# Optimization experiments

Hardware: AMD Instinct MI355X
Metric: run time of the kernel (lower is better)

The kernel has to match this reference:

```python
import jax, jax.numpy as jnp
import numpy as np

D_MODEL = 256
H = 4              # hardcoded in the torch module via repeat(1,4,1)
DIM = D_MODEL // H # 64
N = 4096


def _conv1x1(x, W, b):
    # torch Conv1d(kernel_size=1): [B, Cin, N] -> [B, Cout, N]
    return jnp.einsum('oi,bin->bon', W, x) + b[None, :, None]


def setup_inputs() -> dict:
    key = jax.random.key(0)
    ks = jax.random.split(key, 13)
    s = 0.02
    inp = {
        'query':   jax.random.normal(ks[0], (1, D_MODEL, N), dtype=jnp.float32),
        'key':     jax.random.normal(ks[1], (1, D_MODEL, N), dtype=jnp.float32),
        'value':   jax.random.normal(ks[2], (1, D_MODEL, N), dtype=jnp.float32),
        'coords0': jax.random.normal(ks[3], (1, 3, N), dtype=jnp.float32),
        'coords1': jax.random.normal(ks[4], (1, 3, N), dtype=jnp.float32),
        'Wq': jax.random.normal(ks[5], (D_MODEL, D_MODEL), dtype=jnp.float32) * s,
        'bq': jnp.zeros((D_MODEL,), dtype=jnp.float32),
        'Wk': jax.random.normal(ks[6], (D_MODEL, D_MODEL), dtype=jnp.float32) * s,
        'bk': jnp.zeros((D_MODEL,), dtype=jnp.float32),
        'Wv': jax.random.normal(ks[7], (D_MODEL, D_MODEL), dtype=jnp.float32) * s,
        'bv': jnp.zeros((D_MODEL,), dtype=jnp.float32),
        'Wm': jax.random.normal(ks[8], (D_MODEL + 28, D_MODEL + 28), dtype=jnp.float32) * s,
        'bm': jnp.zeros((D_MODEL + 28,), dtype=jnp.float32),
    }
    return inp


def reference(query, key, value, coords0, coords1, Wq, bq, Wk, bk, Wv, bv, Wm, bm):
    B = query.shape[0]  # must be 1 (hardcoded in original via view(1,4,3,-1))
    Nq = coords0.shape[2]
    Nk = coords1.shape[2]

    # 1x1-conv projections, then split channels into (dim, heads): view(B, dim, H, N)
    q = _conv1x1(query, Wq, bq).reshape(B, DIM, H, Nq)
    k = _conv1x1(key,   Wk, bk).reshape(B, DIM, H, Nk)
    v = _conv1x1(value, Wv, bv).reshape(B, DIM, H, Nk)

    # coords1.repeat(1,4,1).view(1,4,3,-1).transpose(1,2) == broadcast coords over heads
    c1 = jnp.broadcast_to(coords1[:, :, None, :], (B, 3, H, Nk))
    v = jnp.concatenate([v, c1], axis=1)  # [B, DIM+3, H, Nk]

    # attention: scale is query.shape[1]**0.5 == DIM**0.5 (per-head dim)
    scores = jnp.einsum('bdhn,bdhm->bhnm', q, k) / jnp.asarray(DIM, q.dtype) ** 0.5
    prob = jax.nn.softmax(scores, axis=-1)          # [B, H, Nq, Nk]
    x = jnp.einsum('bhnm,bdhm->bdhn', prob, v)      # [B, DIM+3, H, Nq]

    # coordinate augmentation
    c0 = jnp.broadcast_to(coords0[:, :, None, :], (B, 3, H, Nq))
    aug1 = x[:, DIM:DIM + 3] - c0                   # [B, 3, H, Nq]
    aug2 = jnp.linalg.norm(aug1, axis=1, keepdims=True)  # [B, 1, H, Nq]

    y = jnp.concatenate([x, aug1, aug2], axis=1)    # [B, DIM+7, H, Nq]
    y = y.reshape(B, (DIM + 7) * H, Nq)
    return _conv1x1(y, Wm, bm)                      # [B, d_model+28, Nq]
```

## Files before the change

### kernel.cpp

```cpp
#include <hip/hip_runtime.h>
#include <hip/hip_bf16.h>

#define NN 4096

typedef __attribute__((ext_vector_type(8))) short short8;
typedef __attribute__((ext_vector_type(4))) float f32x4;

__device__ __forceinline__ unsigned short f2bf(float f) {
  union { float f; unsigned u; } v; v.f = f;
  unsigned u = v.u;
  u += 0x7fffu + ((u >> 16) & 1u);
  return (unsigned short)(u >> 16);
}

__device__ __forceinline__ unsigned packpair(float a, float b) {
  __hip_bfloat162 h = __float22bfloat162_rn(make_float2(a, b));
  union { __hip_bfloat162 h; unsigned u; } cv; cv.h = h;
  return cv.u;
}

__global__ __launch_bounds__(256) void transpose3_kernel(
    const float* __restrict__ q, const float* __restrict__ k, const float* __restrict__ v,
    unsigned short* __restrict__ Xt, const float* __restrict__ coords1,
    unsigned short* __restrict__ Vb) {
  __shared__ float Tl[64][65];
  const float* X = (blockIdx.z == 0) ? q : (blockIdx.z == 1) ? k : v;
  unsigned short* dst = Xt + (size_t)blockIdx.z * NN * 256;
  const int n0 = blockIdx.x << 6, k0 = blockIdx.y << 6;
  const int t = threadIdx.x;
  const int r = t >> 4, c4 = (t & 15) << 2;
#pragma unroll
  for (int i = 0; i < 4; ++i) {
    const float4 vv = *(const float4*)(X + (size_t)(k0 + r + 16 * i) * NN + n0 + c4);
    Tl[r + 16 * i][c4] = vv.x; Tl[r + 16 * i][c4 + 1] = vv.y;
    Tl[r + 16 * i][c4 + 2] = vv.z; Tl[r + 16 * i][c4 + 3] = vv.w;
  }
  __syncthreads();
  const int kc = (t & 7) << 3;
#pragma unroll
  for (int j = 0; j < 2; ++j) {
    const int n = (t >> 3) + (j << 5);
    unsigned pk[4];
#pragma unroll
    for (int u = 0; u < 4; ++u)
      pk[u] = packpair(Tl[kc + 2 * u][n], Tl[kc + 2 * u + 1][n]);
    *(uint4*)(dst + (size_t)(n0 + n) * 256 + k0 + kc) = *(uint4*)pk;
  }
  if (blockIdx.z == 2 && blockIdx.y == 0) {
    const int rr = t >> 2, seg = t & 3;
    const int h = rr >> 4, d = 64 + (rr & 15);
    unsigned short* vd = Vb + (size_t)(h * 80 + d) * NN + n0 + seg * 16;
    if (d < 67) {
      const float* src = coords1 + (size_t)(d - 64) * NN + n0 + seg * 16;
      unsigned u[8];
#pragma unroll
      for (int i = 0; i < 4; ++i) {
        const float4 cv = *(const float4*)(src + 4 * i);
        u[2 * i] = packpair(cv.x, cv.y);
        u[2 * i + 1] = packpair(cv.z, cv.w);
      }
      *(uint4*)vd = *(uint4*)&u[0];
      *(uint4*)(vd + 8) = *(uint4*)&u[4];
    } else {
      const uint4 zz = make_uint4(0u, 0u, 0u, 0u);
      *(uint4*)vd = zz;
      *(uint4*)(vd + 8) = zz;
    }
  }
}

__global__ __launch_bounds__(256) void proj_gemm_kernel(
    const float* __restrict__ Wq, const float* __restrict__ bq,
    const float* __restrict__ Wk, const float* __restrict__ bk,
    const float* __restrict__ Wv, const float* __restrict__ bv,
    const unsigned short* __restrict__ Xt,
    unsigned short* __restrict__ Qb, unsigned short* __restrict__ Kb,
    unsigned short* __restrict__ Vb) {
  __shared__ __align__(16) unsigned char smem[16384];
  __shared__ float Bls[64];
  const int z = blockIdx.z;
  const float* W  = (z == 0) ? Wq : (z == 1) ? Wk : Wv;
  const float* bb = (z == 0) ? bq : (z == 1) ? bk : bv;
  const unsigned short* Xz = Xt + (size_t)z * NN * 256;
  const int co0 = blockIdx.y << 6;
  const int n0 = blockIdx.x << 6;
  const int tid = threadIdx.x;
  const int w = tid >> 6, l = tid & 63;
  const int wm = w >> 1, wn = w & 1;
  const int c = l & 15, g = l >> 4;
  char* const Al = (char*)smem;
  char* const Bl = (char*)smem + 8192;

  if (tid < 64) Bls[tid] = bb[co0 + tid];

  const int ar = tid >> 2, ac = (tid & 3) << 4;
  const int br = tid >> 3, bch = tid & 7;
  const int aswz = (ar & 7) << 4;
  const int bswz = (br & 7) << 4;

  float4 wa[4];
  uint4 wb[2];
  f32x4 acc[2][2];
#pragma unroll
  for (int mf = 0; mf < 2; ++mf)
#pragma unroll
    for (int nf = 0; nf < 2; ++nf) acc[mf][nf] = (f32x4){0.f, 0.f, 0.f, 0.f};

#define PJ_LOAD(k0_) do { \
  _Pragma("unroll") for (int i = 0; i < 4; ++i) \
    wa[i] = *(const float4*)(W + (size_t)(co0 + ar) * 256 + (k0_) + ac + 4 * i); \
  wb[0] = *(const uint4*)(Xz + (size_t)(n0 + br) * 256 + (k0_) + bch * 8); \
  wb[1] = *(const uint4*)(Xz + (size_t)(n0 + br + 32) * 256 + (k0_) + bch * 8); \
} while (0)

#define PJ_STORE() do { \
  unsigned pk[8]; \
  _Pragma("unroll") for (int i = 0; i < 4; ++i) { \
    pk[2 * i] = packpair(wa[i].x, wa[i].y); \
    pk[2 * i + 1] = packpair(wa[i].z, wa[i].w); \
  } \
  *(uint4*)(Al + ar * 128 + (((ac << 1)) ^ aswz)) = *(uint4*)&pk[0]; \
  *(uint4*)(Al + ar * 128 + (((ac << 1) + 16) ^ aswz)) = *(uint4*)&pk[4]; \
  *(uint4*)(Bl + br * 128 + ((bch << 4) ^ bswz)) = wb[0]; \
  *(uint4*)(Bl + (br + 32) * 128 + ((bch << 4) ^ bswz)) = wb[1]; \
} while (0)

  PJ_LOAD(0);
  PJ_STORE();
  __syncthreads();

  for (int s = 0; s < 4; ++s) {
    const bool hav = (s + 1 < 4);
    if (hav) PJ_LOAD((s + 1) << 6);
    __builtin_amdgcn_s_setprio(1);
#pragma unroll
    for (int ks = 0; ks < 2; ++ks) {
      short8 af[2], bf[2];
#pragma unroll
      for (int mf = 0; mf < 2; ++mf) {
        const int row = wm * 32 + mf * 16 + c;
        af[mf] = *(const short8*)(Al + row * 128 + (((ks << 6) + (g << 4)) ^ ((row & 7) << 4)));
      }
#pragma unroll
      for (int nf = 0; nf < 2; ++nf) {
        const int row = wn * 32 + nf * 16 + c;
        bf[nf] = *(const short8*)(Bl + row * 128 + (((ks << 6) + (g << 4)) ^ ((row & 7) << 4)));
      }
#pragma unroll
      for (int mf = 0; mf < 2; ++mf)
#pragma unroll
        for (int nf = 0; nf < 2; ++nf)
          acc[mf][nf] = __builtin_amdgcn_mfma_f32_16x16x32_bf16(af[mf], bf[nf], acc[mf][nf], 0, 0, 0);
    }
    __builtin_amdgcn_s_setprio(0);
    __syncthreads();
    if (hav) {
      PJ_STORE();
      __syncthreads();
    }
  }

  unsigned short* Clu = (unsigned short*)smem;
  const float scale = (z == 0) ? 0.125f : 1.0f;
#pragma unroll
  for (int mf = 0; mf < 2; ++mf)
#pragma unroll
    for (int nf = 0; nf < 2; ++nf)
#pragma unroll
      for (int rr = 0; rr < 4; ++rr) {
        const int row = wm * 32 + mf * 16 + (g << 2) + rr;
        const int col = wn * 32 + nf * 16 + c;
        Clu[row * 72 + col] = f2bf((acc[mf][nf][rr] + Bls[row]) * scale);
      }
  __syncthreads();
  if (z <= 1) {
    unsigned short* Ob = (z == 0) ? Qb : Kb;
    const int d0 = co0 >> 2;
    const int h = tid >> 6, n = tid & 63;
    unsigned u[8];
#pragma unroll
    for (int p = 0; p < 8; ++p)
      u[p] = (unsigned)Clu[((p << 3) + h) * 72 + n] |
             ((unsigned)Clu[((p << 3) + 4 + h) * 72 + n] << 16);
    uint4* dd = (uint4*)(Ob + ((size_t)h * NN + n0 + n) * 64 + d0);
    dd[0] = *(uint4*)&u[0];
    dd[1] = *(uint4*)&u[4];
  } else {
    const int rl = tid >> 2, seg = (tid & 3) << 4;
    const int h = rl & 3, d = (co0 >> 2) + (rl >> 2);
    unsigned short* vd = Vb + (size_t)(h * 80 + d) * NN + n0 + seg;
    *(uint4*)vd = *(const uint4*)((char*)Clu + rl * 144 + (seg << 1));
    *(uint4*)(vd + 8) = *(const uint4*)((char*)Clu + rl * 144 + (seg << 1) + 16);
  }
}

__global__ __launch_bounds__(256) void attn_kernel(
    const unsigned short* __restrict__ Qb, const unsigned short* __restrict__ Kb,
    const unsigned short* __restrict__ Vb, float* __restrict__ Opart, int chunkKeys) {
  __shared__ __align__(16) unsigned char smem[34816];
  const int h = blockIdx.y;
  const int sp = blockIdx.z;
  const int qbase = blockIdx.x * 128;
  const int tid = threadIdx.x;
  const int w = tid >> 6;
  const int l = tid & 63;
  const int c = l & 15;
  const int g = l >> 4;
  const int swc = (c & 7) << 4;

  char* const Kls = (char*)smem;
  char* const Vls = (char*)smem + 8192;
  char* const Pls = (char*)smem + 18432 + w * 4096;

  short8 qf[2][2];
#pragma unroll
  for (int qs = 0; qs < 2; ++qs) {
    const unsigned short* qsrc = Qb + (((h * NN) + qbase + w * 32 + qs * 16 + c) << 6) + (g << 3);
    qf[qs][0] = *(const short8*)qsrc;
    qf[qs][1] = *(const short8*)(qsrc + 32);
  }

  f32x4 Of[2][5];
#pragma unroll
  for (int qs = 0; qs < 2; ++qs)
#pragma unroll
    for (int dt = 0; dt < 5; ++dt) Of[qs][dt] = (f32x4){0.f, 0.f, 0.f, 0.f};
  float mrun[2] = {-1e30f, -1e30f};
  float lrun[2] = {0.f, 0.f};

  const int r0 = tid >> 3, ch = tid & 7;
  const int so = (ch << 4) ^ ((r0 & 7) << 4);
  const int mStart = sp * chunkKeys;
  const int niter = chunkKeys >> 6;

  {
    const unsigned short* kbase = Kb + ((h * NN + mStart) << 6);
    const unsigned short* vbase = Vb + (size_t)(h * 80) * NN + mStart;
    const uint4 ka  = *(const uint4*)(kbase + (r0 << 6) + (ch << 3));
    const uint4 kb2 = *(const uint4*)(kbase + ((r0 + 32) << 6) + (ch << 3));
    const uint4 va  = *(const uint4*)(vbase + (size_t)r0 * NN + (ch << 3));
    const uint4 vb2 = *(const uint4*)(vbase + (size_t)(r0 + 32) * NN + (ch << 3));
    *(uint4*)(Kls + r0 * 128 + so) = ka;
    *(uint4*)(Kls + (r0 + 32) * 128 + so) = kb2;
    *(uint4*)(Vls + r0 * 128 + so) = va;
    *(uint4*)(Vls + (r0 + 32) * 128 + so) = vb2;
    if (tid < 128) {
      const uint4 vc = *(const uint4*)(vbase + (size_t)(r0 + 64) * NN + (ch << 3));
      *(uint4*)(Vls + (r0 + 64) * 128 + so) = vc;
    }
  }
  __syncthreads();

  for (int it = 0; it < niter; ++it) {
    uint4 ka, kb2, va, vb2, vc;
    const bool hav = (it + 1 < niter);
    if (hav) {
      const int m0 = mStart + ((it + 1) << 6);
      const unsigned short* kbase = Kb + ((h * NN + m0) << 6);
      const unsigned short* vbase = Vb + (size_t)(h * 80) * NN + m0;
      ka  = *(const uint4*)(kbase + (r0 << 6) + (ch << 3));
      kb2 = *(const uint4*)(kbase + ((r0 + 32) << 6) + (ch << 3));
      va  = *(const uint4*)(vbase + (size_t)r0 * NN + (ch << 3));
      vb2 = *(const uint4*)(vbase + (size_t)(r0 + 32) * NN + (ch << 3));
      if (tid < 128) vc = *(const uint4*)(vbase + (size_t)(r0 + 64) * NN + (ch << 3));
    }

    f32x4 sD[2][4];
    __builtin_amdgcn_s_setprio(1);
#pragma unroll
    for (int t = 0; t < 4; ++t) {
      const char* rp = Kls + (t * 16 + c) * 128;
      const short8 ka0 = *(const short8*)(rp + ((g << 4) ^ swc));
      const short8 ka1 = *(const short8*)(rp + ((64 + (g << 4)) ^ swc));
#pragma unroll
      for (int qs = 0; qs < 2; ++qs) {
        f32x4 a = (f32x4){0.f, 0.f, 0.f, 0.f};
        a = __builtin_amdgcn_mfma_f32_16x16x32_bf16(ka0, qf[qs][0], a, 0, 0, 0);
        a = __builtin_amdgcn_mfma_f32_16x16x32_bf16(ka1, qf[qs][1], a, 0, 0, 0);
        sD[qs][t] = a;
      }
    }
    __builtin_amdgcn_s_setprio(0);

#pragma unroll
    for (int qs = 0; qs < 2; ++qs) {
      float m01 = fmaxf(fmaxf(sD[qs][0][0], sD[qs][0][1]), fmaxf(sD[qs][0][2], sD[qs][0][3]));
      float m11 = fmaxf(fmaxf(sD[qs][1][0], sD[qs][1][1]), fmaxf(sD[qs][1][2], sD[qs][1][3]));
      float m21 = fmaxf(fmaxf(sD[qs][2][0], sD[qs][2][1]), fmaxf(sD[qs][2][2], sD[qs][2][3]));
      float m31 = fmaxf(fmaxf(sD[qs][3][0], sD[qs][3][1]), fmaxf(sD[qs][3][2], sD[qs][3][3]));
      float mx = fmaxf(fmaxf(m01, m11), fmaxf(m21, m31));
      mx = fmaxf(mx, __shfl_xor(mx, 16));
      mx = fmaxf(mx, __shfl_xor(mx, 32));
      if (!__all(mx - mrun[qs] <= 8.f)) {
        const float mnew = fmaxf(mrun[qs], mx);
        const float a = __expf(mrun[qs] - mnew);
        mrun[qs] = mnew;
        lrun[qs] *= a;
#pragma unroll
        for (int dt = 0; dt < 5; ++dt)
#pragma unroll
          for (int r = 0; r < 4; ++r) Of[qs][dt][r] *= a;
      }
      const float mm = mrun[qs];
      float rs = 0.f;
      unsigned pk[8];
#pragma unroll
      for (int t = 0; t < 4; ++t) {
        const float e0 = __expf(sD[qs][t][0] - mm);
        const float e1 = __expf(sD[qs][t][1] - mm);
        const float e2 = __expf(sD[qs][t][2] - mm);
        const float e3 = __expf(sD[qs][t][3] - mm);
        rs += (e0 + e1) + (e2 + e3);
        pk[t * 2]     = packpair(e0, e1);
        pk[t * 2 + 1] = packpair(e2, e3);
      }
      rs += __shfl_xor(rs, 16);
      rs += __shfl_xor(rs, 32);
      lrun[qs] += rs;
      char* prow = Pls + (qs * 16 + c) * 128;
#pragma unroll
      for (int t = 0; t < 4; ++t)
        *(uint2*)(prow + ((t * 32 + (g << 3)) ^ swc)) = make_uint2(pk[t * 2], pk[t * 2 + 1]);
    }

    short8 pb[2][2];
#pragma unroll
    for (int qs = 0; qs < 2; ++qs) {
      const char* prow = Pls + (qs * 16 + c) * 128;
      pb[qs][0] = *(const short8*)(prow + ((g << 4) ^ swc));
      pb[qs][1] = *(const short8*)(prow + ((64 + (g << 4)) ^ swc));
    }
    __builtin_amdgcn_s_setprio(1);
#pragma unroll
    for (int dt = 0; dt < 5; ++dt) {
      const char* vp = Vls + (dt * 16 + c) * 128;
      const short8 va0 = *(const short8*)(vp + ((g << 4) ^ swc));
      const short8 va1 = *(const short8*)(vp + ((64 + (g << 4)) ^ swc));
#pragma unroll
      for (int qs = 0; qs < 2; ++qs) {
        Of[qs][dt] = __builtin_amdgcn_mfma_f32_16x16x32_bf16(va0, pb[qs][0], Of[qs][dt], 0, 0, 0);
        Of[qs][dt] = __builtin_amdgcn_mfma_f32_16x16x32_bf16(va1, pb[qs][1], Of[qs][dt], 0, 0, 0);
      }
    }
    __builtin_amdgcn_s_setprio(0);

    __syncthreads();
    if (hav) {
      *(uint4*)(Kls + r0 * 128 + so) = ka;
      *(uint4*)(Kls + (r0 + 32) * 128 + so) = kb2;
      *(uint4*)(Vls + r0 * 128 + so) = va;
      *(uint4*)(Vls + (r0 + 32) * 128 + so) = vb2;
      if (tid < 128) *(uint4*)(Vls + (r0 + 64) * 128 + so) = vc;
    }
    __syncthreads();
  }

  const int rowbase = (sp * 4 + h) * 69;
#pragma unroll
  for (int qs = 0; qs < 2; ++qs) {
    const int qg = qbase + w * 32 + qs * 16 + c;
#pragma unroll
    for (int dt = 0; dt < 5; ++dt)
#pragma unroll
      for (int r = 0; r < 4; ++r) {
        const int dv = dt * 16 + (g << 2) + r;
        if (dv < 67) Opart[(size_t)(rowbase + dv) * NN + qg] = Of[qs][dt][r];
      }
    if (g == 0) {
      Opart[(size_t)(rowbase + 67) * NN + qg] = mrun[qs];
      Opart[(size_t)(rowbase + 68) * NN + qg] = lrun[qs];
    }
  }
}

template <int NS>
__global__ __launch_bounds__(256) void combine_t_kernel(
    const float* __restrict__ Opart, const float* __restrict__ coords0,
    unsigned short* __restrict__ Yt) {
  __shared__ __align__(16) unsigned char Yl[16 * 640];
  const int t = threadIdx.x;
  const int q = t & 15;
  const int worker = t >> 4;
  const int h = worker & 3;
  const int dgrp = worker >> 2;
  const int q0 = blockIdx.x << 4;
  const int qg = q0 + q;
  const int rowb = q * 640;
  const int sw = (q & 7) << 4;

  float m[NS], wgt[NS], lv[NS];
  float M = -1e30f;
#pragma unroll
  for (int s = 0; s < NS; ++s)
    m[s] = Opart[((size_t)(s * 4 + h) * 69 + 67) * NN + qg];
#pragma unroll
  for (int s = 0; s < NS; ++s)
    lv[s] = Opart[((size_t)(s * 4 + h) * 69 + 68) * NN + qg];
#pragma unroll
  for (int s = 0; s < NS; ++s) M = fmaxf(M, m[s]);
  float L = 0.f;
#pragma unroll
  for (int s = 0; s < NS; ++s) {
    wgt[s] = __expf(m[s] - M);
    L += lv[s] * wgt[s];
  }
  const float invL = 1.f / L;
#pragma unroll
  for (int s = 0; s < NS; ++s) wgt[s] *= invL;

  if (worker == 0) *(uint2*)(Yl + rowb + (568 ^ sw)) = make_uint2(0u, 0u);

  const int dv0 = dgrp * 17;
  const int dv1 = (dgrp == 3) ? 67 : dv0 + 17;
  float ss = 0.f;
#pragma unroll 2
  for (int dv = dv0; dv < dv1; ++dv) {
    float vals[NS];
#pragma unroll
    for (int s = 0; s < NS; ++s)
      vals[s] = Opart[((size_t)(s * 4 + h) * 69 + dv) * NN + qg];
    float a = 0.f;
#pragma unroll
    for (int s = 0; s < NS; ++s) a += vals[s] * wgt[s];
    *(unsigned short*)(Yl + rowb + ((((dv << 2) + h) << 1) ^ sw)) = f2bf(a);
    if (dv >= 64) {
      const float au = a - coords0[(size_t)(dv - 64) * NN + qg];
      *(unsigned short*)(Yl + rowb + (((((dv + 3) << 2) + h) << 1) ^ sw)) = f2bf(au);
      ss += au * au;
    }
  }
  if (dgrp == 3) *(unsigned short*)(Yl + rowb + (((280 + h) << 1) ^ sw)) = f2bf(sqrtf(ss));
  __syncthreads();

  for (int i = t; i < 16 * 36; i += 256) {
    const int row = i / 36, seg = i - row * 36;
    *(uint4*)(Yt + (size_t)(q0 + row) * 288 + (seg << 3)) =
        *(const uint4*)(Yl + row * 640 + ((seg << 4) ^ ((row & 7) << 4)));
  }
}

#define OP_LOAD(k0_) do { \
  const int arow = co0 + ar; \
  _Pragma("unroll") for (int i = 0; i < 6; ++i) { \
    const int col = (k0_) + ac + 4 * i; \
    wa[i] = (arow < 284 && col < 284) ? *(const float4*)(Wm + (size_t)arow * 284 + col) \
                                      : make_float4(0.f, 0.f, 0.f, 0.f); \
  } \
  _Pragma("unroll") for (int i = 0; i < 6; ++i) \
    wb[i] = *(const uint4*)(Yt + (size_t)(n0 + bn) * 288 + (k0_) + bc + 8 * i); \
} while (0)

#define OP_WRITE_LDS() do { \
  unsigned pk[12]; \
  _Pragma("unroll") for (int i = 0; i < 6; ++i) { \
    pk[2 * i] = packpair(wa[i].x, wa[i].y); \
    pk[2 * i + 1] = packpair(wa[i].z, wa[i].w); \
  } \
  _Pragma("unroll") for (int i = 0; i < 3; ++i) \
    *(uint4*)(Al + ar * 256 + (((ac << 1) + (i << 4)) ^ aswz)) = *(uint4*)&pk[4 * i]; \
  _Pragma("unroll") for (int i = 0; i < 6; ++i) \
    *(uint4*)(Bl + bn * 256 + (((bc << 1) + (i << 4)) ^ bswz)) = wb[i]; \
} while (0)

__global__ __launch_bounds__(256) void outproj_gemm_kernel(
    const unsigned short* __restrict__ Yt, const float* __restrict__ Wm,
    const float* __restrict__ bm, float* __restrict__ out) {
  __shared__ __align__(16) unsigned char smem[49152];
  __shared__ float Bls[64];
  const int co0 = blockIdx.y << 6;
  const int n0 = blockIdx.x << 7;
  const int tid = threadIdx.x;
  const int w = tid >> 6, l = tid & 63;
  const int wm = w >> 1, wn = w & 1;
  const int c = l & 15, g = l >> 4;
  char* const Al = (char*)smem;
  char* const Bl = (char*)smem + 16384;

  if (tid < 64) { const int co = co0 + tid; Bls[tid] = (co < 284) ? bm[co] : 0.f; }

  const int ar = tid >> 2, ac = (tid & 3) * 24;
  const int bn = tid >> 1, bc = (tid & 1) * 48;
  const int aswz = (ar & 7) << 4;
  const int bswz = (bn & 7) << 4;

  float4 wa[6];
  uint4 wb[6];
  f32x4 acc[2][4];
#pragma unroll
  for (int mf = 0; mf < 2; ++mf)
#pragma unroll
    for (int nf = 0; nf < 4; ++nf) acc[mf][nf] = (f32x4){0.f, 0.f, 0.f, 0.f};

  OP_LOAD(0);
  OP_WRITE_LDS();
  __syncthreads();

  for (int s = 0; s < 3; ++s) {
    const bool hav = (s + 1 < 3);
    if (hav) OP_LOAD((s + 1) * 96);
    __builtin_amdgcn_s_setprio(1);
#pragma unroll
    for (int ks = 0; ks < 3; ++ks) {
      short8 af[2], bf[4];
#pragma unroll
      for (int mf = 0; mf < 2; ++mf) {
        const int row = wm * 32 + mf * 16 + c;
        af[mf] = *(const short8*)(Al + row * 256 + (((ks << 6) + (g << 4)) ^ ((row & 7) << 4)));
      }
#pragma unroll
      for (int nf = 0; nf < 4; ++nf) {
        const int row = wn * 64 + nf * 16 + c;
        bf[nf] = *(const short8*)(Bl + row * 256 + (((ks << 6) + (g << 4)) ^ ((row & 7) << 4)));
      }
#pragma unroll
      for (int mf = 0; mf < 2; ++mf)
#pragma unroll
        for (int nf = 0; nf < 4; ++nf)
          acc[mf][nf] = __builtin_amdgcn_mfma_f32_16x16x32_bf16(af[mf], bf[nf], acc[mf][nf], 0, 0, 0);
    }
    __builtin_amdgcn_s_setprio(0);
    __syncthreads();
    if (hav) {
      OP_WRITE_LDS();
      __syncthreads();
    }
  }

#pragma unroll
  for (int mf = 0; mf < 2; ++mf)
#pragma unroll
    for (int nf = 0; nf < 4; ++nf)
#pragma unroll
      for (int rr = 0; rr < 4; ++rr) {
        const int row = wm * 32 + mf * 16 + (g << 2) + rr;
        const int co = co0 + row;
        if (co < 284)
          out[(size_t)co * NN + n0 + wn * 64 + nf * 16 + c] = acc[mf][nf][rr] + Bls[row];
      }
}

extern "C" void kernel_launch(void* const* d_in, const int* in_sizes, int n_in,
                              void* d_out, int out_size, void* d_ws, size_t ws_size,
                              hipStream_t stream) {
  const float* query   = (const float*)d_in[0];
  const float* key_    = (const float*)d_in[1];
  const float* value   = (const float*)d_in[2];
  const float* coords0 = (const float*)d_in[3];
  const float* coords1 = (const float*)d_in[4];
  const float* Wq = (const float*)d_in[5];
  const float* bq = (const float*)d_in[6];
  const float* Wk = (const float*)d_in[7];
  const float* bk = (const float*)d_in[8];
  const float* Wv = (const float*)d_in[9];
  const float* bv = (const float*)d_in[10];
  const float* Wm = (const float*)d_in[11];
  const float* bm = (const float*)d_in[12];
  float* out = (float*)d_out;

  unsigned short* Qb = (unsigned short*)d_ws;
  unsigned short* Kb = Qb + (size_t)4 * NN * 64;
  unsigned short* Vb = Kb + (size_t)4 * NN * 64;
  unsigned short* Xt = Vb + (size_t)4 * 80 * NN;
  unsigned short* Yt = Xt + (size_t)3 * NN * 256;
  float* Opart = (float*)(Yt + (size_t)NN * 288);

  const size_t fixedB = (size_t)((char*)Opart - (char*)d_ws);
  const size_t per = (size_t)4 * 69 * NN * 4;
  int nsplit = 8;
  while (nsplit > 1 && ws_size < fixedB + (size_t)nsplit * per) nsplit >>= 1;

  hipLaunchKernelGGL(transpose3_kernel, dim3(64, 4, 3), dim3(256), 0, stream,
                     query, key_, value, Xt, coords1, Vb);
  hipLaunchKernelGGL(proj_gemm_kernel, dim3(64, 4, 3), dim3(256), 0, stream,
                     Wq, bq, Wk, bk, Wv, bv, Xt, Qb, Kb, Vb);
  hipLaunchKernelGGL(attn_kernel, dim3(32, 4, nsplit), dim3(256), 0, stream,
                     Qb, Kb, Vb, Opart, NN / nsplit);
  switch (nsplit) {
    case 8:
      hipLaunchKernelGGL((combine_t_kernel<8>), dim3(256), dim3(256), 0, stream, Opart, coords0, Yt);
      break;
    case 4:
      hipLaunchKernelGGL((combine_t_kernel<4>), dim3(256), dim3(256), 0, stream, Opart, coords0, Yt);
      break;
    case 2:
      hipLaunchKernelGGL((combine_t_kernel<2>), dim3(256), dim3(256), 0, stream, Opart, coords0, Yt);
      break;
    default:
      hipLaunchKernelGGL((combine_t_kernel<1>), dim3(256), dim3(256), 0, stream, Opart, coords0, Yt);
      break;
  }
  hipLaunchKernelGGL(outproj_gemm_kernel, dim3(32, 5), dim3(256), 0, stream, Yt, Wm, bm, out);
}
```

Before: 93.47 us.

## Double-buffer attention K/V tiles, use exp2 softmax, shrink out-proj tile

The attention kernel now alternates between two LDS buffers for its K/V tiles. This removes one __syncthreads per iteration but raises shared memory per block, which may cut occupancy. The softmax folds log2(e) into the Q scale and uses the hardware exp2 instruction in place of __expf, with the rescale threshold widened to match the base-2 units. The output projection GEMM tile width is halved to 64 columns, doubling the grid so more blocks run across CUs.

```diff
diff --git a/kernel.cpp b/kernel.cpp
--- a/kernel.cpp
+++ b/kernel.cpp
@@ -161,7 +161,7 @@
   }
 
   unsigned short* Clu = (unsigned short*)smem;
-  const float scale = (z == 0) ? 0.125f : 1.0f;
+  const float scale = (z == 0) ? 0.18033688f : 1.0f;
 #pragma unroll
   for (int mf = 0; mf < 2; ++mf)
 #pragma unroll
@@ -197,7 +197,7 @@
 __global__ __launch_bounds__(256) void attn_kernel(
     const unsigned short* __restrict__ Qb, const unsigned short* __restrict__ Kb,
     const unsigned short* __restrict__ Vb, float* __restrict__ Opart, int chunkKeys) {
-  __shared__ __align__(16) unsigned char smem[34816];
+  __shared__ __align__(16) unsigned char smem[53248];
   const int h = blockIdx.y;
   const int sp = blockIdx.z;
   const int qbase = blockIdx.x * 128;
@@ -208,9 +208,7 @@
   const int g = l >> 4;
   const int swc = (c & 7) << 4;
 
-  char* const Kls = (char*)smem;
-  char* const Vls = (char*)smem + 8192;
-  char* const Pls = (char*)smem + 18432 + w * 4096;
+  char* const Pls = (char*)smem + 36864 + w * 4096;
 
   short8 qf[2][2];
 #pragma unroll
@@ -234,6 +232,8 @@
   const int niter = chunkKeys >> 6;
 
   {
+    char* const Kls = (char*)smem;
+    char* const Vls = (char*)smem + 8192;
     const unsigned short* kbase = Kb + ((h * NN + mStart) << 6);
     const unsigned short* vbase = Vb + (size_t)(h * 80) * NN + mStart;
     const uint4 ka  = *(const uint4*)(kbase + (r0 << 6) + (ch << 3));
@@ -252,6 +252,11 @@
   __syncthreads();
 
   for (int it = 0; it < niter; ++it) {
+    char* const KlsC = (char*)smem + ((it & 1) ? 18432 : 0);
+    char* const VlsC = KlsC + 8192;
+    char* const KlsN = (char*)smem + ((it & 1) ? 0 : 18432);
+    char* const VlsN = KlsN + 8192;
+
     uint4 ka, kb2, va, vb2, vc;
     const bool hav = (it + 1 < niter);
     if (hav) {
@@ -269,7 +274,7 @@
     __builtin_amdgcn_s_setprio(1);
 #pragma unroll
     for (int t = 0; t < 4; ++t) {
-      const char* rp = Kls + (t * 16 + c) * 128;
+      const char* rp = KlsC + (t * 16 + c) * 128;
       const short8 ka0 = *(const short8*)(rp + ((g << 4) ^ swc));
       const short8 ka1 = *(const short8*)(rp + ((64 + (g << 4)) ^ swc));
 #pragma unroll
@@ -291,9 +296,9 @@
       float mx = fmaxf(fmaxf(m01, m11), fmaxf(m21, m31));
       mx = fmaxf(mx, __shfl_xor(mx, 16));
       mx = fmaxf(mx, __shfl_xor(mx, 32));
-      if (!__all(mx - mrun[qs] <= 8.f)) {
+      if (!__all(mx - mrun[qs] <= 11.5f)) {
         const float mnew = fmaxf(mrun[qs], mx);
-        const float a = __expf(mrun[qs] - mnew);
+        const float a = __builtin_amdgcn_exp2f(mrun[qs] - mnew);
         mrun[qs] = mnew;
         lrun[qs] *= a;
 #pragma unroll
@@ -306,10 +311,10 @@
       unsigned pk[8];
 #pragma unroll
       for (int t = 0; t < 4; ++t) {
-        const float e0 = __expf(sD[qs][t][0] - mm);
-        const float e1 = __expf(sD[qs][t][1] - mm);
-        const float e2 = __expf(sD[qs][t][2] - mm);
-        const float e3 = __expf(sD[qs][t][3] - mm);
+        const float e0 = __builtin_amdgcn_exp2f(sD[qs][t][0] - mm);
+        const float e1 = __builtin_amdgcn_exp2f(sD[qs][t][1] - mm);
+        const float e2 = __builtin_amdgcn_exp2f(sD[qs][t][2] - mm);
+        const float e3 = __builtin_amdgcn_exp2f(sD[qs][t][3] - mm);
         rs += (e0 + e1) + (e2 + e3);
         pk[t * 2]     = packpair(e0, e1);
         pk[t * 2 + 1] = packpair(e2, e3);
@@ -333,7 +338,7 @@
     __builtin_amdgcn_s_setprio(1);
 #pragma unroll
     for (int dt = 0; dt < 5; ++dt) {
-      const char* vp = Vls + (dt * 16 + c) * 128;
+      const char* vp = VlsC + (dt * 16 + c) * 128;
       const short8 va0 = *(const short8*)(vp + ((g << 4) ^ swc));
       const short8 va1 = *(const short8*)(vp + ((64 + (g << 4)) ^ swc));
 #pragma unroll
@@ -344,13 +349,12 @@
     }
     __builtin_amdgcn_s_setprio(0);
 
-    __syncthreads();
     if (hav) {
-      *(uint4*)(Kls + r0 * 128 + so) = ka;
-      *(uint4*)(Kls + (r0 + 32) * 128 + so) = kb2;
-      *(uint4*)(Vls + r0 * 128 + so) = va;
-      *(uint4*)(Vls + (r0 + 32) * 128 + so) = vb2;
-      if (tid < 128) *(uint4*)(Vls + (r0 + 64) * 128 + so) = vc;
+      *(uint4*)(KlsN + r0 * 128 + so) = ka;
+      *(uint4*)(KlsN + (r0 + 32) * 128 + so) = kb2;
+      *(uint4*)(VlsN + r0 * 128 + so) = va;
+      *(uint4*)(VlsN + (r0 + 32) * 128 + so) = vb2;
+      if (tid < 128) *(uint4*)(VlsN + (r0 + 64) * 128 + so) = vc;
     }
     __syncthreads();
   }
@@ -401,7 +405,7 @@
   float L = 0.f;
 #pragma unroll
   for (int s = 0; s < NS; ++s) {
-    wgt[s] = __expf(m[s] - M);
+    wgt[s] = __builtin_amdgcn_exp2f(m[s] - M);
     L += lv[s] * wgt[s];
   }
   const float invL = 1.f / L;
@@ -446,7 +450,7 @@
     wa[i] = (arow < 284 && col < 284) ? *(const float4*)(Wm + (size_t)arow * 284 + col) \
                                       : make_float4(0.f, 0.f, 0.f, 0.f); \
   } \
-  _Pragma("unroll") for (int i = 0; i < 6; ++i) \
+  _Pragma("unroll") for (int i = 0; i < 3; ++i) \
     wb[i] = *(const uint4*)(Yt + (size_t)(n0 + bn) * 288 + (k0_) + bc + 8 * i); \
 } while (0)
 
@@ -458,17 +462,17 @@
   } \
   _Pragma("unroll") for (int i = 0; i < 3; ++i) \
     *(uint4*)(Al + ar * 256 + (((ac << 1) + (i << 4)) ^ aswz)) = *(uint4*)&pk[4 * i]; \
-  _Pragma("unroll") for (int i = 0; i < 6; ++i) \
+  _Pragma("unroll") for (int i = 0; i < 3; ++i) \
     *(uint4*)(Bl + bn * 256 + (((bc << 1) + (i << 4)) ^ bswz)) = wb[i]; \
 } while (0)
 
 __global__ __launch_bounds__(256) void outproj_gemm_kernel(
     const unsigned short* __restrict__ Yt, const float* __restrict__ Wm,
     const float* __restrict__ bm, float* __restrict__ out) {
-  __shared__ __align__(16) unsigned char smem[49152];
+  __shared__ __align__(16) unsigned char smem[32768];
   __shared__ float Bls[64];
   const int co0 = blockIdx.y << 6;
-  const int n0 = blockIdx.x << 7;
+  const int n0 = blockIdx.x << 6;
   const int tid = threadIdx.x;
   const int w = tid >> 6, l = tid & 63;
   const int wm = w >> 1, wn = w & 1;
@@ -479,17 +483,17 @@
   if (tid < 64) { const int co = co0 + tid; Bls[tid] = (co < 284) ? bm[co] : 0.f; }
 
   const int ar = tid >> 2, ac = (tid & 3) * 24;
-  const int bn = tid >> 1, bc = (tid & 1) * 48;
+  const int bn = tid >> 2, bc = (tid & 3) * 24;
   const int aswz = (ar & 7) << 4;
   const int bswz = (bn & 7) << 4;
 
   float4 wa[6];
-  uint4 wb[6];
-  f32x4 acc[2][4];
+  uint4 wb[3];
+  f32x4 acc[2][2];
 #pragma unroll
   for (int mf = 0; mf < 2; ++mf)
 #pragma unroll
-    for (int nf = 0; nf < 4; ++nf) acc[mf][nf] = (f32x4){0.f, 0.f, 0.f, 0.f};
+    for (int nf = 0; nf < 2; ++nf) acc[mf][nf] = (f32x4){0.f, 0.f, 0.f, 0.f};
 
   OP_LOAD(0);
   OP_WRITE_LDS();
@@ -501,21 +505,21 @@
     __builtin_amdgcn_s_setprio(1);
 #pragma unroll
     for (int ks = 0; ks < 3; ++ks) {
-      short8 af[2], bf[4];
+      short8 af[2], bf[2];
 #pragma unroll
       for (int mf = 0; mf < 2; ++mf) {
         const int row = wm * 32 + mf * 16 + c;
         af[mf] = *(const short8*)(Al + row * 256 + (((ks << 6) + (g << 4)) ^ ((row & 7) << 4)));
       }
 #pragma unroll
-      for (int nf = 0; nf < 4; ++nf) {
-        const int row = wn * 64 + nf * 16 + c;
+      for (int nf = 0; nf < 2; ++nf) {
+        const int row = wn * 32 + nf * 16 + c;
         bf[nf] = *(const short8*)(Bl + row * 256 + (((ks << 6) + (g << 4)) ^ ((row & 7) << 4)));
       }
 #pragma unroll
       for (int mf = 0; mf < 2; ++mf)
 #pragma unroll
-        for (int nf = 0; nf < 4; ++nf)
+        for (int nf = 0; nf < 2; ++nf)
           acc[mf][nf] = __builtin_amdgcn_mfma_f32_16x16x32_bf16(af[mf], bf[nf], acc[mf][nf], 0, 0, 0);
     }
     __builtin_amdgcn_s_setprio(0);
@@ -529,13 +533,13 @@
 #pragma unroll
   for (int mf = 0; mf < 2; ++mf)
 #pragma unroll
-    for (int nf = 0; nf < 4; ++nf)
+    for (int nf = 0; nf < 2; ++nf)
 #pragma unroll
       for (int rr = 0; rr < 4; ++rr) {
         const int row = wm * 32 + mf * 16 + (g << 2) + rr;
         const int co = co0 + row;
         if (co < 284)
-          out[(size_t)co * NN + n0 + wn * 64 + nf * 16 + c] = acc[mf][nf][rr] + Bls[row];
+          out[(size_t)co * NN + n0 + wn * 32 + nf * 16 + c] = acc[mf][nf][rr] + Bls[row];
       }
 }
 
@@ -589,5 +593,5 @@
       hipLaunchKernelGGL((combine_t_kernel<1>), dim3(256), dim3(256), 0, stream, Opart, coords0, Yt);
       break;
   }
-  hipLaunchKernelGGL(outproj_gemm_kernel, dim3(32, 5), dim3(256), 0, stream, Yt, Wm, bm, out);
-}
+  hipLaunchKernelGGL(outproj_gemm_kernel, dim3(64, 5), dim3(256), 0, stream, Yt, Wm, bm, out);
+}
```

Result: faster. 90.59 us (-3.1%).
